# Kernel optimization log

Hardware: AMD Instinct MI355X
Metric: run time of the kernel (lower is better)

The kernel has to match this reference:

```python
import jax, jax.numpy as jnp
import numpy as np

N_SUPPORT = 32768
N_QUERY = 16384
D = 512
K = 32
U = 128
NEG_BIG = -1e30  # masked-out attention logit; all-masked class -> uniform weights == mean fallback


def setup_inputs() -> dict:
    key = jax.random.key(0)
    k1, k2, k3, k4, k5 = jax.random.split(key, 5)
    query = jax.random.normal(k1, (N_QUERY, D), dtype=jnp.float32)
    support = jax.random.normal(k2, (N_SUPPORT, D), dtype=jnp.float32)
    labels = jax.random.randint(k3, (N_SUPPORT,), 0, K, dtype=jnp.int32)
    # Xavier-normal-ish init for per-class projection V (U,D) and attention vector w (U,1)
    V = jax.random.normal(k4, (K, U, D), dtype=jnp.float32) * np.float32(np.sqrt(2.0 / (U + D)))
    w = jax.random.normal(k5, (K, U), dtype=jnp.float32) * np.float32(np.sqrt(2.0 / (U + 1)))
    return {"query_embeddings": query, "support_embeddings": support,
            "support_labels": labels, "V": V, "w": w}


def reference(query_embeddings, support_embeddings, support_labels, V, w):
    # --- attention-weighted prototypes (vectorized over classes via masked softmax) ---
    # projected[k,n,u] = tanh(V[k] @ x_n)
    projected = jnp.tanh(jnp.einsum('nd,kud->knu', support_embeddings, V))
    attn_logits = jnp.einsum('knu,ku->kn', projected, w)              # (K, N)
    mask = support_labels[None, :] == jnp.arange(K, dtype=support_labels.dtype)[:, None]
    attn_logits = jnp.where(mask, attn_logits, NEG_BIG)
    # per-class softmax over support samples; an empty class yields uniform weights,
    # i.e. prototype = mean(embeddings) -- exactly the torch fallback branch.
    attn = jax.nn.softmax(attn_logits, axis=1)                        # (K, N)
    prototypes = jnp.einsum('kn,nd->kd', attn, support_embeddings)    # (K, D)

    # --- squared-euclidean distance classification ---
    q2 = jnp.sum(query_embeddings * query_embeddings, axis=1, keepdims=True)   # (B, 1)
    p2 = jnp.sum(prototypes * prototypes, axis=1)[None, :]                     # (1, K)
    dists = q2 + p2 - 2.0 * (query_embeddings @ prototypes.T)                  # (B, K)
    return jax.nn.log_softmax(-dists, axis=1)
```

## Files before the change

kernel.cpp:

```cpp
#include <hip/hip_runtime.h>
#include <hip/hip_bf16.h>

#define N_SUPPORT 32768
#define N_QUERY   16384
#define DIM       512
#define NCLS      32
#define NU        128
#define NBLK      (N_SUPPORT / 256)

#define OFF_IDX      0
#define OFF_COUNT    131072
#define OFF_START    131200
#define OFF_M        131456
#define OFF_Z        131584
#define OFF_P2       131712
#define OFF_LOGIT    132096
#define OFF_PRAW     263168
#define OFF_PROTO    328704
#define OFF_BHIST    394240
#define OFF_BOFFS    410624
#define OFF_VBF      458752
#define OFF_PBF      4653056

typedef __attribute__((ext_vector_type(8))) short short8;
typedef __attribute__((ext_vector_type(4))) short short4v;
typedef __attribute__((ext_vector_type(4))) float f32x4;

__device__ inline unsigned short f2bf(float f) {
    unsigned int x = __builtin_bit_cast(unsigned int, f);
    unsigned int r = x + 0x7fffu + ((x >> 16) & 1u);
    return (unsigned short)(r >> 16);
}
__device__ inline float bf2f(unsigned short h) {
    unsigned int u = ((unsigned int)h) << 16;
    return __builtin_bit_cast(float, u);
}

__device__ inline short8 pack_bf8(float4 f0, float4 f1) {
    short8 pk;
    pk[0] = f2bf(f0.x); pk[1] = f2bf(f0.y); pk[2] = f2bf(f0.z); pk[3] = f2bf(f0.w);
    pk[4] = f2bf(f1.x); pk[5] = f2bf(f1.y); pk[6] = f2bf(f1.z); pk[7] = f2bf(f1.w);
    return pk;
}

__device__ inline void pack_hilo(float4 f0, float4 f1, short8& hi, short8& lo) {
    float v[8] = {f0.x, f0.y, f0.z, f0.w, f1.x, f1.y, f1.z, f1.w};
    #pragma unroll
    for (int i = 0; i < 8; i++) {
        unsigned short h = f2bf(v[i]);
        hi[i] = (short)h;
        lo[i] = (short)f2bf(v[i] - bf2f(h));
    }
}

__global__ void k_vcast(const float* __restrict__ V, short* __restrict__ Vbf,
                        float* __restrict__ praw, const int* __restrict__ labels,
                        int* __restrict__ bhist) {
    __shared__ int h[NCLS];
    int tid = threadIdx.x;
    bool dohist = (blockIdx.x < NBLK);
    if (dohist) {
        if (tid < NCLS) h[tid] = 0;
        __syncthreads();
        atomicAdd(&h[labels[blockIdx.x * 256 + tid]], 1);
    }
    int i = blockIdx.x * 256 + tid;
    int ob = i * 4;
    int j0  = ob & 7;
    int s   = (ob >> 3) & 7;
    int u   = (ob >> 6) & 127;
    int c   = (ob >> 13) & 7;
    int k   = ob >> 16;
    int d   = c * 64 + ((s ^ (u & 7)) * 8) + j0;
    float4 f = *(const float4*)(V + ((size_t)(k * 128 + u) * DIM + d));
    short4v o;
    o[0] = f2bf(f.x); o[1] = f2bf(f.y); o[2] = f2bf(f.z); o[3] = f2bf(f.w);
    *(short4v*)(Vbf + (size_t)ob) = o;
    if (i < (NCLS * DIM) / 4) *(float4*)(praw + i * 4) = make_float4(0.f, 0.f, 0.f, 0.f);
    if (dohist) {
        __syncthreads();
        if (tid < NCLS) bhist[blockIdx.x * NCLS + tid] = h[tid];
    }
}

__global__ void k_scan2(const int* __restrict__ bhist, int* __restrict__ boffs,
                        int* __restrict__ start, int* __restrict__ count) {
    __shared__ int tot[NCLS];
    int tid = threadIdx.x;
    if (tid < NCLS) {
        int s = 0;
        for (int b = 0; b < NBLK; b++) {
            boffs[b * NCLS + tid] = s;
            s += bhist[b * NCLS + tid];
        }
        tot[tid] = s;
    }
    __syncthreads();
    if (tid == 0) {
        int run = 0;
        for (int k = 0; k < NCLS; k++) {
            start[k] = run;
            count[k] = tot[k];
            run += tot[k];
        }
        start[NCLS] = run;
    }
}

__global__ void k_scatter(const int* __restrict__ labels, const int* __restrict__ boffs,
                          const int* __restrict__ start, int* __restrict__ idx_c) {
    __shared__ int whist[4][NCLS];
    int tid = threadIdx.x;
    int n = blockIdx.x * 256 + tid;
    int l = labels[n];
    int lane = tid & 63, wid = tid >> 6;
    unsigned long long mymask = 0ull;
    #pragma unroll
    for (int k = 0; k < NCLS; k++) {
        unsigned long long mk = __ballot(l == k);
        if (k == l) mymask = mk;
        if (lane == k) whist[wid][k] = __popcll(mk);
    }
    int rank = __popcll(mymask & ((1ull << lane) - 1ull));
    __syncthreads();
    int wbase = 0;
    for (int w = 0; w < wid; w++) wbase += whist[w][l];
    idx_c[start[l] + boffs[blockIdx.x * NCLS + l] + wbase + rank] = n;
}

__launch_bounds__(512, 1)
__global__ void k_logits(const float* __restrict__ support, const short* __restrict__ Vbf,
                         const float* __restrict__ w, const int* __restrict__ idx_c,
                         const int* __restrict__ start, const int* __restrict__ count,
                         float* __restrict__ logit_c) {
    int k = blockIdx.y;
    int cnt = count[k];
    int base = blockIdx.x * 64;
    if (base >= cnt) return;
    int M = min(64, cnt - base);
    int s0 = start[k] + base;
    int t = threadIdx.x;

    __shared__ __align__(16) short Xs[2][64 * 64];
    __shared__ __align__(16) short Vs[2][128 * 64];
    __shared__ float part[8][64];
    __shared__ int sidx[64];
    if (t < 64) sidx[t] = idx_c[s0 + ((t < M) ? t : 0)];
    __syncthreads();

    int l = t & 63, wv = t >> 6;
    int lo16 = l & 15, hi4 = l >> 4;

    int xrow = t >> 3, xslot = t & 7;
    int xdst = xrow * 64 + ((xslot ^ (xrow & 7)) * 8);
    const float* xsrc = support + (size_t)sidx[xrow] * DIM + xslot * 8;
    const short* Vkc = Vbf + (size_t)k * (8 * 128 * 64);

    f32x4 acc[4];
    #pragma unroll
    for (int mt = 0; mt < 4; mt++) acc[mt] = (f32x4){0.f, 0.f, 0.f, 0.f};

    float4 xa0, xa1, xb0, xb1, xc0, xc1;
    short8 va[2], vb[2], vc[2];

#define LOADX(d0, d1, c) { d0 = *(const float4*)(xsrc + (c) * 64); \
                           d1 = *(const float4*)(xsrc + (c) * 64 + 4); }
#define LOADV(dst, c) { _Pragma("unroll") for (int rep = 0; rep < 2; rep++)   \
        dst[rep] = *(const short8*)(Vkc + (size_t)(c) * 8192 + (size_t)(t + 512 * rep) * 8); }
#define WRITEB(buf, x0, x1, vs) { *(short8*)&Xs[buf][xdst] = pack_bf8(x0, x1); \
        _Pragma("unroll") for (int rep = 0; rep < 2; rep++)                    \
        *(short8*)&Vs[buf][(t + 512 * rep) * 8] = vs[rep]; }
#define MFMA_CHUNK(cur) { _Pragma("unroll")                                       \
    for (int ks = 0; ks < 2; ks++) {                                              \
        short8 a[4], b;                                                           \
        _Pragma("unroll")                                                         \
        for (int mt = 0; mt < 4; mt++) {                                          \
            int ar = mt * 16 + lo16;                                              \
            a[mt] = *(short8*)&Xs[cur][ar * 64 + (((ks * 4 + hi4) ^ (ar & 7)) * 8)]; \
        }                                                                         \
        int vr = wv * 16 + lo16;                                                  \
        b = *(short8*)&Vs[cur][vr * 64 + (((ks * 4 + hi4) ^ (vr & 7)) * 8)];      \
        _Pragma("unroll")                                                         \
        for (int mt = 0; mt < 4; mt++)                                            \
            acc[mt] = __builtin_amdgcn_mfma_f32_16x16x32_bf16(a[mt], b, acc[mt], 0, 0, 0); \
    } }
#define BAR() { asm volatile("s_waitcnt lgkmcnt(0)" ::: "memory"); __builtin_amdgcn_s_barrier(); }

    LOADX(xa0, xa1, 0); LOADV(va, 0);
    LOADX(xb0, xb1, 1); LOADV(vb, 1);
    LOADX(xc0, xc1, 2); LOADV(vc, 2);
    WRITEB(0, xa0, xa1, va);

    BAR(); LOADX(xa0, xa1, 3); LOADV(va, 3); MFMA_CHUNK(0); WRITEB(1, xb0, xb1, vb);
    BAR(); LOADX(xb0, xb1, 4); LOADV(vb, 4); MFMA_CHUNK(1); WRITEB(0, xc0, xc1, vc);
    BAR(); LOADX(xc0, xc1, 5); LOADV(vc, 5); MFMA_CHUNK(0); WRITEB(1, xa0, xa1, va);
    BAR(); LOADX(xa0, xa1, 6); LOADV(va, 6); MFMA_CHUNK(1); WRITEB(0, xb0, xb1, vb);
    BAR(); LOADX(xb0, xb1, 7); LOADV(vb, 7); MFMA_CHUNK(0); WRITEB(1, xc0, xc1, vc);
    BAR(); MFMA_CHUNK(1); WRITEB(0, xa0, xa1, va);
    BAR(); MFMA_CHUNK(0); WRITEB(1, xb0, xb1, vb);
    BAR(); MFMA_CHUNK(1);

#undef LOADX
#undef LOADV
#undef WRITEB
#undef MFMA_CHUNK
#undef BAR

    float wval = w[k * NU + wv * 16 + lo16];
    #pragma unroll
    for (int mt = 0; mt < 4; mt++) {
        #pragma unroll
        for (int r = 0; r < 4; r++) {
            float val = tanhf(acc[mt][r]) * wval;
            val += __shfl_xor(val, 1);
            val += __shfl_xor(val, 2);
            val += __shfl_xor(val, 4);
            val += __shfl_xor(val, 8);
            if (lo16 == 0) part[wv][mt * 16 + hi4 * 4 + r] = val;
        }
    }
    __syncthreads();
    if (t < 64 && t < M) {
        float s = 0.f;
        #pragma unroll
        for (int wq = 0; wq < 8; wq++) s += part[wq][t];
        logit_c[s0 + t] = s;
    }
}

__global__ void k_mz(const float* __restrict__ logit_c, const int* __restrict__ start,
                     const int* __restrict__ count, float* __restrict__ m, float* __restrict__ Z) {
    int k = blockIdx.x;
    int cnt = count[k], s0 = start[k];
    int tid = threadIdx.x;
    __shared__ float red[256];
    float mx = -1e30f;
    for (int i = tid; i < cnt; i += 256) mx = fmaxf(mx, logit_c[s0 + i]);
    red[tid] = mx; __syncthreads();
    for (int off = 128; off > 0; off >>= 1) {
        if (tid < off) red[tid] = fmaxf(red[tid], red[tid + off]);
        __syncthreads();
    }
    float mk = red[0];
    __syncthreads();
    float s = 0.f;
    for (int i = tid; i < cnt; i += 256) s += expf(logit_c[s0 + i] - mk);
    red[tid] = s; __syncthreads();
    for (int off = 128; off > 0; off >>= 1) {
        if (tid < off) red[tid] += red[tid + off];
        __syncthreads();
    }
    if (tid == 0) { m[k] = mk; Z[k] = red[0]; }
}

__launch_bounds__(512, 1)
__global__ void k_proto(const float* __restrict__ support, const int* __restrict__ idx_c,
                        const float* __restrict__ logit_c, const int* __restrict__ start,
                        const int* __restrict__ count, const float* __restrict__ m,
                        float* __restrict__ praw) {
    int k = blockIdx.y;
    int cnt = count[k];
    int base = blockIdx.x * 64;
    if (base >= cnt) return;
    int M = min(64, cnt - base);
    int s0 = start[k] + base;
    __shared__ float wts[64];
    __shared__ int sid[64];
    int t = threadIdx.x;
    if (t < 64) {
        sid[t] = idx_c[s0 + ((t < M) ? t : 0)];
        wts[t] = (t < M) ? expf(logit_c[s0 + t] - m[k]) : 0.f;
    }
    __syncthreads();
    int d = t;
    float a = 0.f;
    for (int s = 0; s < 64; s += 4) {
        float r0 = support[(size_t)sid[s + 0] * DIM + d];
        float r1 = support[(size_t)sid[s + 1] * DIM + d];
        float r2 = support[(size_t)sid[s + 2] * DIM + d];
        float r3 = support[(size_t)sid[s + 3] * DIM + d];
        a += wts[s] * r0 + wts[s + 1] * r1 + wts[s + 2] * r2 + wts[s + 3] * r3;
    }
    atomicAdd(&praw[k * DIM + d], a);
}

__global__ void k_protonorm(const float* __restrict__ support, const float* __restrict__ praw,
                            const float* __restrict__ Z, const int* __restrict__ count,
                            float* __restrict__ proto, float* __restrict__ p2,
                            short* __restrict__ Pbf) {
    int k = blockIdx.x;
    int tid = threadIdx.x;
    int cnt = count[k];
    __shared__ float red[256];
    float pv[2];
    if (cnt > 0) {
        float inv = 1.f / Z[k];
        #pragma unroll
        for (int i = 0; i < 2; i++) pv[i] = praw[k * DIM + tid + i * 256] * inv;
    } else {
        #pragma unroll
        for (int i = 0; i < 2; i++) {
            int d = tid + i * 256;
            float s = 0.f;
            for (int n = 0; n < N_SUPPORT; n++) s += support[(size_t)n * DIM + d];
            pv[i] = s * (1.f / N_SUPPORT);
        }
    }
    float acc = 0.f;
    #pragma unroll
    for (int i = 0; i < 2; i++) {
        int d = tid + i * 256;
        proto[k * DIM + d] = pv[i];
        acc += pv[i] * pv[i];
        int c = d >> 6, off = d & 63, o = off >> 3, j = off & 7;
        int s = o ^ (k & 7);
        int pos = (c * 32 + k) * 64 + s * 8 + j;
        unsigned short hi = f2bf(pv[i]);
        Pbf[pos] = (short)hi;
        Pbf[NCLS * DIM + pos] = (short)f2bf(pv[i] - bf2f(hi));
    }
    red[tid] = acc; __syncthreads();
    for (int off = 128; off > 0; off >>= 1) {
        if (tid < off) red[tid] += red[tid + off];
        __syncthreads();
    }
    if (tid == 0) p2[k] = red[0];
}

__launch_bounds__(256, 1)
__global__ void k_dist(const float* __restrict__ query, const short* __restrict__ Pbf,
                       const float* __restrict__ p2, float* __restrict__ out) {
    __shared__ __align__(16) short Ph[NCLS * DIM];
    __shared__ __align__(16) short Pl[NCLS * DIM];
    __shared__ __align__(16) short Qh[2][64 * 64];
    __shared__ __align__(16) short Ql[2][64 * 64];
    int t = threadIdx.x;
    int qbase = blockIdx.x * 64;
    int l = t & 63, wv = t >> 6;
    int lo16 = l & 15, hi4 = l >> 4;

    #pragma unroll
    for (int rep = 0; rep < 8; rep++) {
        int u = t + 256 * rep;
        ((short8*)Ph)[u] = ((const short8*)Pbf)[u];
        ((short8*)Pl)[u] = ((const short8*)(Pbf + NCLS * DIM))[u];
    }

    int qrow[2], qslot[2], qdst[2];
    const float* qsrc[2];
    #pragma unroll
    for (int rep = 0; rep < 2; rep++) {
        int u = t + 256 * rep;
        qrow[rep] = u >> 3; qslot[rep] = u & 7;
        qdst[rep] = qrow[rep] * 64 + ((qslot[rep] ^ (qrow[rep] & 7)) * 8);
        qsrc[rep] = query + (size_t)(qbase + qrow[rep]) * DIM + qslot[rep] * 8;
    }

    f32x4 acc[2];
    acc[0] = (f32x4){0.f, 0.f, 0.f, 0.f};
    acc[1] = (f32x4){0.f, 0.f, 0.f, 0.f};

    float4 qa[2][2], qb[2][2];
#define LOADQ(d, c) { _Pragma("unroll") for (int rep = 0; rep < 2; rep++) { \
        d[rep][0] = *(const float4*)(qsrc[rep] + (c) * 64);                 \
        d[rep][1] = *(const float4*)(qsrc[rep] + (c) * 64 + 4); } }
#define WRITEQ(buf, d) { _Pragma("unroll") for (int rep = 0; rep < 2; rep++) { \
        short8 hi8, lo8;                                                        \
        pack_hilo(d[rep][0], d[rep][1], hi8, lo8);                              \
        *(short8*)&Qh[buf][qdst[rep]] = hi8;                                    \
        *(short8*)&Ql[buf][qdst[rep]] = lo8; } }

    LOADQ(qa, 0);
    LOADQ(qb, 1);
    WRITEQ(0, qa);

    for (int c = 0; c < 8; ++c) {
        int cur = c & 1;
        __syncthreads();
        if (c + 2 < 8) {
            if (cur == 0) { LOADQ(qa, c + 2); }
            else          { LOADQ(qb, c + 2); }
        }
        #pragma unroll
        for (int ks = 0; ks < 2; ks++) {
            int arow = wv * 16 + lo16;
            int asw = ((ks * 4 + hi4) ^ (arow & 7)) * 8;
            short8 ah = *(short8*)&Qh[cur][arow * 64 + asw];
            short8 al = *(short8*)&Ql[cur][arow * 64 + asw];
            #pragma unroll
            for (int nt = 0; nt < 2; nt++) {
                int brow = nt * 16 + lo16;
                int pos = (c * 32 + brow) * 64 + (((ks * 4 + hi4) ^ (brow & 7)) * 8);
                short8 bh = *(short8*)&Ph[pos];
                short8 bl = *(short8*)&Pl[pos];
                acc[nt] = __builtin_amdgcn_mfma_f32_16x16x32_bf16(ah, bh, acc[nt], 0, 0, 0);
                acc[nt] = __builtin_amdgcn_mfma_f32_16x16x32_bf16(ah, bl, acc[nt], 0, 0, 0);
                acc[nt] = __builtin_amdgcn_mfma_f32_16x16x32_bf16(al, bh, acc[nt], 0, 0, 0);
            }
        }
        if (c < 7) {
            if (cur == 0) { WRITEQ(1, qb); }
            else          { WRITEQ(0, qa); }
        }
    }
#undef LOADQ
#undef WRITEQ

    float p2v0 = p2[lo16];
    float p2v1 = p2[16 + lo16];
    #pragma unroll
    for (int r = 0; r < 4; r++) {
        float l0 = 2.f * acc[0][r] - p2v0;
        float l1 = 2.f * acc[1][r] - p2v1;
        float mx = fmaxf(l0, l1);
        mx = fmaxf(mx, __shfl_xor(mx, 1));
        mx = fmaxf(mx, __shfl_xor(mx, 2));
        mx = fmaxf(mx, __shfl_xor(mx, 4));
        mx = fmaxf(mx, __shfl_xor(mx, 8));
        float s = expf(l0 - mx) + expf(l1 - mx);
        s += __shfl_xor(s, 1);
        s += __shfl_xor(s, 2);
        s += __shfl_xor(s, 4);
        s += __shfl_xor(s, 8);
        float lse = mx + logf(s);
        int q = qbase + wv * 16 + hi4 * 4 + r;
        out[(size_t)q * NCLS + lo16] = l0 - lse;
        out[(size_t)q * NCLS + 16 + lo16] = l1 - lse;
    }
}

extern "C" void kernel_launch(void* const* d_in, const int* in_sizes, int n_in,
                              void* d_out, int out_size, void* d_ws, size_t ws_size,
                              hipStream_t stream) {
    const float* query   = (const float*)d_in[0];
    const float* support = (const float*)d_in[1];
    const int*   labels  = (const int*)d_in[2];
    const float* V       = (const float*)d_in[3];
    const float* w       = (const float*)d_in[4];
    float* out = (float*)d_out;
    char* ws = (char*)d_ws;

    int*   idx_c   = (int*)(ws + OFF_IDX);
    int*   count   = (int*)(ws + OFF_COUNT);
    int*   start   = (int*)(ws + OFF_START);
    float* m       = (float*)(ws + OFF_M);
    float* Z       = (float*)(ws + OFF_Z);
    float* p2      = (float*)(ws + OFF_P2);
    float* logit_c = (float*)(ws + OFF_LOGIT);
    float* praw    = (float*)(ws + OFF_PRAW);
    float* proto   = (float*)(ws + OFF_PROTO);
    int*   bhist   = (int*)(ws + OFF_BHIST);
    int*   boffs   = (int*)(ws + OFF_BOFFS);
    short* vbf     = (short*)(ws + OFF_VBF);
    short* pbf     = (short*)(ws + OFF_PBF);

    hipLaunchKernelGGL(k_vcast, dim3((NCLS * NU * DIM) / 1024), dim3(256), 0, stream,
                       V, vbf, praw, labels, bhist);
    hipLaunchKernelGGL(k_scan2, dim3(1), dim3(64), 0, stream, bhist, boffs, start, count);
    hipLaunchKernelGGL(k_scatter, dim3(NBLK), dim3(256), 0, stream, labels, boffs, start, idx_c);
    hipLaunchKernelGGL(k_logits, dim3(32, NCLS), dim3(512), 0, stream,
                       support, vbf, w, idx_c, start, count, logit_c);
    hipLaunchKernelGGL(k_mz, dim3(NCLS), dim3(256), 0, stream, logit_c, start, count, m, Z);
    hipLaunchKernelGGL(k_proto, dim3(32, NCLS), dim3(512), 0, stream,
                       support, idx_c, logit_c, start, count, m, praw);
    hipLaunchKernelGGL(k_protonorm, dim3(NCLS), dim3(256), 0, stream,
                       support, praw, Z, count, proto, p2, pbf);
    hipLaunchKernelGGL(k_dist, dim3(N_QUERY / 64), dim3(256), 0, stream, query, pbf, p2, out);
}
```

Before: 70.82 us.

## Split logits kernel over U halves with atomic accumulation of partial logits

The per-class logits kernel is split along the U=128 projection dimension into two 64-wide halves via a third grid dimension, each block running 256 threads instead of 512. Partial weighted-tanh sums are combined with atomicAdd into logit_c, which is now zeroed inside the V-cast kernel. This doubles the number of blocks and halves the per-block LDS footprint to raise occupancy and parallelism. In exchange, each support row is loaded and converted to bf16 twice, and float atomics make the summation order nondeterministic.

```diff
diff --git a/kernel.cpp b/kernel.cpp
--- a/kernel.cpp
+++ b/kernel.cpp
@@ -54,8 +54,8 @@
 }
 
 __global__ void k_vcast(const float* __restrict__ V, short* __restrict__ Vbf,
-                        float* __restrict__ praw, const int* __restrict__ labels,
-                        int* __restrict__ bhist) {
+                        float* __restrict__ praw, float* __restrict__ logit_c,
+                        const int* __restrict__ labels, int* __restrict__ bhist) {
     __shared__ int h[NCLS];
     int tid = threadIdx.x;
     bool dohist = (blockIdx.x < NBLK);
@@ -77,6 +77,7 @@
     o[0] = f2bf(f.x); o[1] = f2bf(f.y); o[2] = f2bf(f.z); o[3] = f2bf(f.w);
     *(short4v*)(Vbf + (size_t)ob) = o;
     if (i < (NCLS * DIM) / 4) *(float4*)(praw + i * 4) = make_float4(0.f, 0.f, 0.f, 0.f);
+    if (i < N_SUPPORT / 4)    *(float4*)(logit_c + i * 4) = make_float4(0.f, 0.f, 0.f, 0.f);
     if (dohist) {
         __syncthreads();
         if (tid < NCLS) bhist[blockIdx.x * NCLS + tid] = h[tid];
@@ -128,12 +129,13 @@
     idx_c[start[l] + boffs[blockIdx.x * NCLS + l] + wbase + rank] = n;
 }
 
-__launch_bounds__(512, 1)
+__launch_bounds__(256, 1)
 __global__ void k_logits(const float* __restrict__ support, const short* __restrict__ Vbf,
                          const float* __restrict__ w, const int* __restrict__ idx_c,
                          const int* __restrict__ start, const int* __restrict__ count,
                          float* __restrict__ logit_c) {
     int k = blockIdx.y;
+    int z = blockIdx.z;
     int cnt = count[k];
     int base = blockIdx.x * 64;
     if (base >= cnt) return;
@@ -142,8 +144,8 @@
     int t = threadIdx.x;
 
     __shared__ __align__(16) short Xs[2][64 * 64];
-    __shared__ __align__(16) short Vs[2][128 * 64];
-    __shared__ float part[8][64];
+    __shared__ __align__(16) short Vs[2][64 * 64];
+    __shared__ float part[4][64];
     __shared__ int sidx[64];
     if (t < 64) sidx[t] = idx_c[s0 + ((t < M) ? t : 0)];
     __syncthreads();
@@ -151,25 +153,32 @@
     int l = t & 63, wv = t >> 6;
     int lo16 = l & 15, hi4 = l >> 4;
 
-    int xrow = t >> 3, xslot = t & 7;
-    int xdst = xrow * 64 + ((xslot ^ (xrow & 7)) * 8);
-    const float* xsrc = support + (size_t)sidx[xrow] * DIM + xslot * 8;
-    const short* Vkc = Vbf + (size_t)k * (8 * 128 * 64);
+    int xdst[2];
+    const float* xsrc[2];
+    #pragma unroll
+    for (int rep = 0; rep < 2; rep++) {
+        int u = t + 256 * rep;
+        int xrow = u >> 3, xslot = u & 7;
+        xdst[rep] = xrow * 64 + ((xslot ^ (xrow & 7)) * 8);
+        xsrc[rep] = support + (size_t)sidx[xrow] * DIM + xslot * 8;
+    }
+    const short* Vkz = Vbf + (size_t)k * (8 * 128 * 64) + z * (64 * 64);
 
     f32x4 acc[4];
     #pragma unroll
     for (int mt = 0; mt < 4; mt++) acc[mt] = (f32x4){0.f, 0.f, 0.f, 0.f};
 
-    float4 xa0, xa1, xb0, xb1, xc0, xc1;
+    float4 xa[2][2], xb[2][2], xc[2][2];
     short8 va[2], vb[2], vc[2];
 
-#define LOADX(d0, d1, c) { d0 = *(const float4*)(xsrc + (c) * 64); \
-                           d1 = *(const float4*)(xsrc + (c) * 64 + 4); }
+#define LOADX(dst, c) { _Pragma("unroll") for (int rep = 0; rep < 2; rep++) { \
+        dst[rep][0] = *(const float4*)(xsrc[rep] + (c) * 64);                 \
+        dst[rep][1] = *(const float4*)(xsrc[rep] + (c) * 64 + 4); } }
 #define LOADV(dst, c) { _Pragma("unroll") for (int rep = 0; rep < 2; rep++)   \
-        dst[rep] = *(const short8*)(Vkc + (size_t)(c) * 8192 + (size_t)(t + 512 * rep) * 8); }
-#define WRITEB(buf, x0, x1, vs) { *(short8*)&Xs[buf][xdst] = pack_bf8(x0, x1); \
-        _Pragma("unroll") for (int rep = 0; rep < 2; rep++)                    \
-        *(short8*)&Vs[buf][(t + 512 * rep) * 8] = vs[rep]; }
+        dst[rep] = *(const short8*)(Vkz + (size_t)(c) * 8192 + (size_t)(t + 256 * rep) * 8); }
+#define WRITEB(buf, xs_, vs_) { _Pragma("unroll") for (int rep = 0; rep < 2; rep++) { \
+        *(short8*)&Xs[buf][xdst[rep]] = pack_bf8(xs_[rep][0], xs_[rep][1]);            \
+        *(short8*)&Vs[buf][(t + 256 * rep) * 8] = vs_[rep]; } }
 #define MFMA_CHUNK(cur) { _Pragma("unroll")                                       \
     for (int ks = 0; ks < 2; ks++) {                                              \
         short8 a[4], b;                                                           \
@@ -186,18 +195,18 @@
     } }
 #define BAR() { asm volatile("s_waitcnt lgkmcnt(0)" ::: "memory"); __builtin_amdgcn_s_barrier(); }
 
-    LOADX(xa0, xa1, 0); LOADV(va, 0);
-    LOADX(xb0, xb1, 1); LOADV(vb, 1);
-    LOADX(xc0, xc1, 2); LOADV(vc, 2);
-    WRITEB(0, xa0, xa1, va);
-
-    BAR(); LOADX(xa0, xa1, 3); LOADV(va, 3); MFMA_CHUNK(0); WRITEB(1, xb0, xb1, vb);
-    BAR(); LOADX(xb0, xb1, 4); LOADV(vb, 4); MFMA_CHUNK(1); WRITEB(0, xc0, xc1, vc);
-    BAR(); LOADX(xc0, xc1, 5); LOADV(vc, 5); MFMA_CHUNK(0); WRITEB(1, xa0, xa1, va);
-    BAR(); LOADX(xa0, xa1, 6); LOADV(va, 6); MFMA_CHUNK(1); WRITEB(0, xb0, xb1, vb);
-    BAR(); LOADX(xb0, xb1, 7); LOADV(vb, 7); MFMA_CHUNK(0); WRITEB(1, xc0, xc1, vc);
-    BAR(); MFMA_CHUNK(1); WRITEB(0, xa0, xa1, va);
-    BAR(); MFMA_CHUNK(0); WRITEB(1, xb0, xb1, vb);
+    LOADX(xa, 0); LOADV(va, 0);
+    LOADX(xb, 1); LOADV(vb, 1);
+    LOADX(xc, 2); LOADV(vc, 2);
+    WRITEB(0, xa, va);
+
+    BAR(); LOADX(xa, 3); LOADV(va, 3); MFMA_CHUNK(0); WRITEB(1, xb, vb);
+    BAR(); LOADX(xb, 4); LOADV(vb, 4); MFMA_CHUNK(1); WRITEB(0, xc, vc);
+    BAR(); LOADX(xc, 5); LOADV(vc, 5); MFMA_CHUNK(0); WRITEB(1, xa, va);
+    BAR(); LOADX(xa, 6); LOADV(va, 6); MFMA_CHUNK(1); WRITEB(0, xb, vb);
+    BAR(); LOADX(xb, 7); LOADV(vb, 7); MFMA_CHUNK(0); WRITEB(1, xc, vc);
+    BAR(); MFMA_CHUNK(1); WRITEB(0, xa, va);
+    BAR(); MFMA_CHUNK(0); WRITEB(1, xb, vb);
     BAR(); MFMA_CHUNK(1);
 
 #undef LOADX
@@ -206,7 +215,7 @@
 #undef MFMA_CHUNK
 #undef BAR
 
-    float wval = w[k * NU + wv * 16 + lo16];
+    float wval = w[k * NU + z * 64 + wv * 16 + lo16];
     #pragma unroll
     for (int mt = 0; mt < 4; mt++) {
         #pragma unroll
@@ -221,10 +230,8 @@
     }
     __syncthreads();
     if (t < 64 && t < M) {
-        float s = 0.f;
-        #pragma unroll
-        for (int wq = 0; wq < 8; wq++) s += part[wq][t];
-        logit_c[s0 + t] = s;
+        float s = part[0][t] + part[1][t] + part[2][t] + part[3][t];
+        atomicAdd(&logit_c[s0 + t], s);
     }
 }
 
@@ -455,10 +462,10 @@
     short* pbf     = (short*)(ws + OFF_PBF);
 
     hipLaunchKernelGGL(k_vcast, dim3((NCLS * NU * DIM) / 1024), dim3(256), 0, stream,
-                       V, vbf, praw, labels, bhist);
+                       V, vbf, praw, logit_c, labels, bhist);
     hipLaunchKernelGGL(k_scan2, dim3(1), dim3(64), 0, stream, bhist, boffs, start, count);
     hipLaunchKernelGGL(k_scatter, dim3(NBLK), dim3(256), 0, stream, labels, boffs, start, idx_c);
-    hipLaunchKernelGGL(k_logits, dim3(32, NCLS), dim3(512), 0, stream,
+    hipLaunchKernelGGL(k_logits, dim3(32, NCLS, 2), dim3(256), 0, stream,
                        support, vbf, w, idx_c, start, count, logit_c);
     hipLaunchKernelGGL(k_mz, dim3(NCLS), dim3(256), 0, stream, logit_c, start, count, m, Z);
     hipLaunchKernelGGL(k_proto, dim3(32, NCLS), dim3(512), 0, stream,
```

After: 76.60 us. +8.2%, slower.
